# Optimization experiments

Hardware: AMD Instinct MI355X
Metric: run time of the kernel (lower is better)

Reference implementation:

```python
import jax, jax.numpy as jnp
import numpy as np

N, E, D_IN, D_OUT = 50000, 300000, 256, 256
BN_EPS = 1e-5


def ccorr(a, b):
    # circular correlation: irfft(conj(rfft(a)) * rfft(b))
    return jnp.fft.irfft(jnp.conj(jnp.fft.rfft(a, axis=-1)) * jnp.fft.rfft(b, axis=-1), n=a.shape[-1], axis=-1)


def setup_inputs() -> dict:
    key = jax.random.key(0)
    ks = jax.random.split(key, 8)
    return {
        "node_ft": jax.random.normal(ks[0], (N, D_IN), dtype=jnp.float32),
        "edge_ft": jax.random.normal(ks[1], (E, D_IN), dtype=jnp.float32),
        "norm": jax.random.uniform(ks[2], (N, 1), dtype=jnp.float32),
        "w_loop": jax.random.normal(ks[3], (D_IN, D_OUT), dtype=jnp.float32) * (1.414 / np.sqrt(D_IN)),
        "w_in": jax.random.normal(ks[4], (D_IN, D_OUT), dtype=jnp.float32) * (1.414 / np.sqrt(D_IN)),
        "loop_rel": jax.random.normal(ks[5], (1, D_IN), dtype=jnp.float32),
        "w_bias": jnp.zeros((D_OUT,), dtype=jnp.float32),
        "bn_gamma": jnp.ones((D_OUT,), dtype=jnp.float32),
        "bn_beta": jnp.zeros((D_OUT,), dtype=jnp.float32),
        "src": jax.random.randint(ks[6], (E,), 0, N, dtype=jnp.int32),
        "dst": jax.random.randint(ks[7], (E,), 0, N, dtype=jnp.int32),
    }


def reference(node_ft, edge_ft, norm, w_loop, w_in, loop_rel, w_bias, bn_gamma, bn_beta, src, dst):
    n_nodes = node_ft.shape[0]
    # self-loop message: ccorr(ft, loop_rel) @ w_loop  [N, d_out]
    loop_msg = ccorr(node_ft, loop_rel) @ w_loop
    # per-edge message: ccorr(src_ft, edge_ft) @ w_in  [E, d_out]
    msg = ccorr(node_ft[src], edge_ft) @ w_in
    # scatter-sum aggregation then norm multiply (apply_func)
    agg = jax.ops.segment_sum(msg, dst, num_segments=n_nodes) * norm
    h = agg + w_bias + loop_msg
    # BatchNorm1d (training mode: batch stats, biased variance)
    mean = jnp.mean(h, axis=0)
    var = jnp.var(h, axis=0)
    h = (h - mean) * jax.lax.rsqrt(var + BN_EPS) * bn_gamma + bn_beta
    return jnp.tanh(h)
```

## Files before the change

kernel.cpp:

```cpp
#include <hip/hip_runtime.h>
#include <hip/hip_bf16.h>

#define NN 50000
#define EE 300000
#define BN_EPS 1e-5f
#define NFW 288
#define TWOPI_256 0.024543692606170259f

typedef __attribute__((ext_vector_type(8))) _Float16 half8;
typedef __attribute__((ext_vector_type(2))) _Float16 half2v;
typedef __attribute__((ext_vector_type(4))) float f32x4;
#define MFMA16F __builtin_amdgcn_mfma_f32_16x16x32_f16

__device__ __align__(16) _Float16 g_NF[(size_t)NN * NFW];
__device__ float g_Wle[256 * 256];
__device__ __align__(16) unsigned short g_FB[8 * 20 * 64 * 8];
__device__ __align__(16) unsigned short g_CB[9 * 16 * 64 * 8];
__device__ __align__(16) unsigned short g_WLEB[8 * 16 * 64 * 8];
__device__ int g_hist[NN];
__device__ int g_off[NN];
__device__ int g_cursor[NN];
__device__ int g_perm[EE];
__device__ int g_bsum[128];
__device__ int g_bbase[128];

__device__ __forceinline__ void atomAddF(float* p, float v) { unsafeAtomicAdd(p, v); }

__device__ __forceinline__ unsigned short f2hu(float x) {
    union { _Float16 f; unsigned short u; } c;
    c.f = (_Float16)x;
    return c.u;
}

__device__ __forceinline__ void stage_write(char* A, const float4* stg, int t) {
#pragma unroll
    for (int q = 0; q < 8; ++q) {
        int idx = q * 512 + t;
        int row = idx >> 6, c4 = idx & 63;
        union { _Float16 f[4]; ushort4 u; } r;
        r.f[0] = (_Float16)stg[q].x; r.f[1] = (_Float16)stg[q].y;
        r.f[2] = (_Float16)stg[q].z; r.f[3] = (_Float16)stg[q].w;
        int ks = c4 >> 3;
        int off = ((row >> 4) * 8 + ks) * 1024 +
                  ((((((c4 >> 1) & 3) << 4) | (row & 15)) * 16) ^ (ks << 4)) +
                  (c4 & 1) * 8;
        *(ushort4*)(A + off) = r.u;
    }
}

__global__ __launch_bounds__(512) void hist_kernel(const int* __restrict__ dst, int E) {
    int e = blockIdx.x * 512 + threadIdx.x;
    if (e < E) atomicAdd(&g_hist[dst[e]], 1);
}

__global__ __launch_bounds__(512) void scanA_kernel(int N) {
    __shared__ int arr[512];
    int t = threadIdx.x, b = blockIdx.x * 512 + t;
    int cnt = (b < N) ? g_hist[b] : 0;
    arr[t] = cnt;
    __syncthreads();
#pragma unroll
    for (int off = 1; off < 512; off <<= 1) {
        int v = (t >= off) ? arr[t - off] : 0;
        __syncthreads();
        arr[t] += v;
        __syncthreads();
    }
    if (b < N) g_off[b] = arr[t] - cnt;
    if (t == 511) g_bsum[blockIdx.x] = arr[511];
}

__global__ __launch_bounds__(128) void scanB_kernel(int nblk) {
    __shared__ int arr[128];
    int t = threadIdx.x;
    int v0 = (t < nblk) ? g_bsum[t] : 0;
    arr[t] = v0;
    __syncthreads();
#pragma unroll
    for (int off = 1; off < 128; off <<= 1) {
        int v = (t >= off) ? arr[t - off] : 0;
        __syncthreads();
        arr[t] += v;
        __syncthreads();
    }
    if (t < nblk) g_bbase[t] = arr[t] - v0;
}

__global__ __launch_bounds__(512) void scanC_kernel(int N) {
    int b = blockIdx.x * 512 + threadIdx.x;
    if (b < N) {
        int v = g_off[b] + g_bbase[blockIdx.x];
        g_off[b] = v;
        g_cursor[b] = v;
    }
}

__global__ __launch_bounds__(512) void perm_kernel(const int* __restrict__ dst, int E) {
    int e = blockIdx.x * 512 + threadIdx.x;
    if (e < E) {
        int pos = atomicAdd(&g_cursor[dst[e]], 1);
        g_perm[pos] = e;
    }
}

__global__ __launch_bounds__(256) void wle_kernel(
    const float* __restrict__ loop_rel, const float* __restrict__ w_loop,
    float* __restrict__ W_le) {
    __shared__ float lr[256];
    const int d = threadIdx.x, j = blockIdx.x;
    lr[d] = loop_rel[d];
    __syncthreads();
    float acc = 0.f;
#pragma unroll 4
    for (int k = 0; k < 256; ++k)
        acc = fmaf(lr[(j + k) & 255], w_loop[k * 256 + d], acc);
    W_le[j * 256 + d] = acc;
}

__global__ __launch_bounds__(512) void fb_pack() {
    int b = blockIdx.x, ks = b / 20, nt = b % 20;
    int t = threadIdx.x, lane = t >> 3, e = t & 7;
    int k = 32 * ks + 8 * (lane >> 4) + e;
    int r2 = nt * 16 + (lane & 15);
    float val = 0.f;
    if (r2 < 258) {
        int f = r2 >> 1;
        int m = (f * k) & 255;
        float s, c;
        sincosf((float)m * TWOPI_256, &s, &c);
        val = (r2 & 1) ? -s : c;
    }
    g_FB[((ks * 20 + nt) * 64 + lane) * 8 + e] = f2hu(val);
}

__global__ __launch_bounds__(512) void cb_pack(const float* __restrict__ w_in) {
    __shared__ float ct[256], st[256];
    int t = threadIdx.x;
    if (t < 256) {
        float s, c;
        sincosf((float)t * TWOPI_256, &s, &c);
        ct[t] = c; st[t] = s;
    }
    __syncthreads();
    int b = blockIdx.x, ks = b / 16, nt = b % 16;
    int lane = t >> 3, e = t & 7;
    int kk = 32 * ks + 8 * (lane >> 4) + e;
    int d = nt * 16 + (lane & 15);
    float val = 0.f;
    if (kk < 258) {
        int f = kk >> 1;
        float cf = (f == 0 || f == 128) ? (1.f / 256.f) : (2.f / 256.f);
        const float* tab = (kk & 1) ? st : ct;
        float sgn = (kk & 1) ? -1.f : 1.f;
        float acc = 0.f;
        for (int k = 0; k < 256; ++k)
            acc = fmaf(tab[(f * k) & 255], w_in[k * 256 + d], acc);
        val = cf * sgn * acc;
    }
    g_CB[((ks * 16 + nt) * 64 + lane) * 8 + e] = f2hu(val);
}

__global__ __launch_bounds__(512) void wleb_pack() {
    int b = blockIdx.x, ks = b / 16, nt = b % 16;
    int t = threadIdx.x, lane = t >> 3, e = t & 7;
    int k = 32 * ks + 8 * (lane >> 4) + e;
    int d = nt * 16 + (lane & 15);
    g_WLEB[((ks * 16 + nt) * 64 + lane) * 8 + e] = f2hu(g_Wle[k * 256 + d]);
}

__global__ __launch_bounds__(512, 4) void nfloop_kernel(
    const float* __restrict__ node_ft, const float* __restrict__ w_bias,
    float* __restrict__ out, int N) {
    __shared__ char smem[32768];
    unsigned short* A = (unsigned short*)smem;
    const int t = threadIdx.x;
    const long long r0 = (long long)blockIdx.x * 64;
    {
        float4 stg[8];
#pragma unroll
        for (int q = 0; q < 8; ++q) {
            int idx = q * 512 + t;
            long long gr = r0 + (idx >> 6);
            if (gr >= N) gr = N - 1;
            stg[q] = ((const float4*)node_ft)[gr * 64 + (idx & 63)];
        }
        stage_write(smem, stg, t);
    }
    __syncthreads();

    const int lane = t & 63, w = t >> 6;
    const int mw = w >> 2, nw = w & 3;
    const int l15 = lane & 15, lg = lane >> 4;

    {
        f32x4 acc[2][5] = {};
#pragma unroll
        for (int ks = 0; ks < 8; ++ks) {
            half8 a0 = *(const half8*)((char*)A + ((2 * mw + 0) * 8 + ks) * 1024 + ((lane * 16) ^ (ks << 4)));
            half8 a1 = *(const half8*)((char*)A + ((2 * mw + 1) * 8 + ks) * 1024 + ((lane * 16) ^ (ks << 4)));
#pragma unroll
            for (int j = 0; j < 4; ++j) {
                int tn = nw + 4 * j;
                half8 bf = *(const half8*)(g_FB + ((size_t)(ks * 20 + tn) * 64 + lane) * 8);
                acc[0][j] = MFMA16F(a0, bf, acc[0][j], 0, 0, 0);
                acc[1][j] = MFMA16F(a1, bf, acc[1][j], 0, 0, 0);
            }
            if (nw == 0) {
                half8 bf = *(const half8*)(g_FB + ((size_t)(ks * 20 + 16) * 64 + lane) * 8);
                acc[0][4] = MFMA16F(a0, bf, acc[0][4], 0, 0, 0);
                acc[1][4] = MFMA16F(a1, bf, acc[1][4], 0, 0, 0);
            }
        }
#pragma unroll
        for (int mt = 0; mt < 2; ++mt)
#pragma unroll
            for (int j = 0; j < 5; ++j) {
                int tn = nw + 4 * j;
                if (tn > 16 || (j == 4 && nw != 0)) continue;
                int r2 = tn * 16 + l15;
#pragma unroll
                for (int r = 0; r < 4; ++r) {
                    long long gr = r0 + (2 * mw + mt) * 16 + lg * 4 + r;
                    if (gr < N && r2 < 258)
                        g_NF[gr * NFW + r2] = (_Float16)acc[mt][j][r];
                }
            }
    }
    {
        f32x4 acc[2][4] = {};
#pragma unroll
        for (int ks = 0; ks < 8; ++ks) {
            half8 a0 = *(const half8*)((char*)A + ((2 * mw + 0) * 8 + ks) * 1024 + ((lane * 16) ^ (ks << 4)));
            half8 a1 = *(const half8*)((char*)A + ((2 * mw + 1) * 8 + ks) * 1024 + ((lane * 16) ^ (ks << 4)));
#pragma unroll
            for (int j = 0; j < 4; ++j) {
                half8 bf = *(const half8*)(g_WLEB + ((size_t)(ks * 16 + 4 * nw + j) * 64 + lane) * 8);
                acc[0][j] = MFMA16F(a0, bf, acc[0][j], 0, 0, 0);
                acc[1][j] = MFMA16F(a1, bf, acc[1][j], 0, 0, 0);
            }
        }
#pragma unroll
        for (int j = 0; j < 4; ++j) {
            const int col = (4 * nw + j) * 16 + l15;
            const float bj = w_bias[col];
#pragma unroll
            for (int mt = 0; mt < 2; ++mt)
#pragma unroll
                for (int r = 0; r < 4; ++r) {
                    long long gr = r0 + (2 * mw + mt) * 16 + lg * 4 + r;
                    if (gr < N)
                        out[gr * 256 + col] = acc[mt][j][r] + bj;
                }
        }
    }
}

__global__ __launch_bounds__(512, 4) void edge_kernel(
    const float* __restrict__ edge_ft, const float* __restrict__ norm,
    const int* __restrict__ src, const int* __restrict__ dst,
    float* __restrict__ agg, int E) {
    __shared__ char smem[36864 + 512];
    unsigned short* A = (unsigned short*)smem;
    unsigned short* Z = (unsigned short*)smem;
    int* sdd = (int*)(smem + 36864);
    float* snrm = (float*)(smem + 36864 + 256);

    const int t = threadIdx.x;
    const long long ebase = (long long)blockIdx.x * 64;
    const int lane = t & 63, w = t >> 6;
    const int mw = w >> 2, nw = w & 3;
    const int l15 = lane & 15, lg = lane >> 4;
    const bool odd = (l15 & 1);

    int srcv[2][4];
#pragma unroll
    for (int mt = 0; mt < 2; ++mt)
#pragma unroll
        for (int r = 0; r < 4; ++r) {
            long long ge = ebase + (2 * mw + mt) * 16 + lg * 4 + r;
            if (ge >= E) ge = E - 1;
            srcv[mt][r] = src[g_perm[ge]];
        }

    if (t < 64) {
        long long ge = ebase + t;
        if (ge >= E) ge = E - 1;
        int d = dst[g_perm[ge]];
        sdd[t] = d;
        snrm[t] = norm[d];
    }

    float4 stg[8];
#pragma unroll
    for (int q = 0; q < 8; ++q) {
        long long ge = ebase + q * 8 + (t >> 6);
        if (ge >= E) ge = E - 1;
        stg[q] = ((const float4*)edge_ft)[(long long)g_perm[ge] * 64 + (t & 63)];
    }

    unsigned int pf[2][5][4];
#pragma unroll
    for (int mt = 0; mt < 2; ++mt)
#pragma unroll
        for (int j = 0; j < 5; ++j) {
            int tn = nw + 4 * j;
            if (tn >= 17) continue;
            int r2 = tn * 16 + l15;
            if (r2 < 258) {
#pragma unroll
                for (int r = 0; r < 4; ++r)
                    pf[mt][j][r] = *(const unsigned int*)(g_NF +
                        (long long)srcv[mt][r] * NFW + (r2 & ~1));
            }
        }
    stage_write(smem, stg, t);
    __syncthreads();

    f32x4 acc1[2][5] = {};
#pragma unroll
    for (int ks = 0; ks < 8; ++ks) {
        half8 a0 = *(const half8*)((char*)A + ((2 * mw + 0) * 8 + ks) * 1024 + ((lane * 16) ^ (ks << 4)));
        half8 a1 = *(const half8*)((char*)A + ((2 * mw + 1) * 8 + ks) * 1024 + ((lane * 16) ^ (ks << 4)));
#pragma unroll
        for (int j = 0; j < 4; ++j) {
            int tn = nw + 4 * j;
            half8 bf = *(const half8*)(g_FB + ((size_t)(ks * 20 + tn) * 64 + lane) * 8);
            acc1[0][j] = MFMA16F(a0, bf, acc1[0][j], 0, 0, 0);
            acc1[1][j] = MFMA16F(a1, bf, acc1[1][j], 0, 0, 0);
        }
        if (nw == 0) {
            half8 bf = *(const half8*)(g_FB + ((size_t)(ks * 20 + 16) * 64 + lane) * 8);
            acc1[0][4] = MFMA16F(a0, bf, acc1[0][4], 0, 0, 0);
            acc1[1][4] = MFMA16F(a1, bf, acc1[1][4], 0, 0, 0);
        }
    }
    __syncthreads();

#pragma unroll
    for (int mt = 0; mt < 2; ++mt) {
        int tm = 2 * mw + mt;
#pragma unroll
        for (int j = 0; j < 5; ++j) {
            int tn = nw + 4 * j;
            if (tn >= 18) continue;
            int r2 = tn * 16 + l15;
#pragma unroll
            for (int r = 0; r < 4; ++r) {
                int e = tm * 16 + lg * 4 + r;
                float z = 0.f;
                if (r2 < 258) {
                    float own = acc1[mt][j][r];
                    float oth = __shfl_xor(own, 1);
                    union { unsigned int u; half2v h; } cv;
                    cv.u = pf[mt][j][r];
                    float br = (float)cv.h[0], bi = (float)cv.h[1];
                    z = odd ? (br * own - bi * oth) : (br * own + bi * oth);
                }
                int ksz = r2 >> 5;
                int off = ((e >> 4) * 9 + ksz) * 1024 +
                          ((((((r2 >> 3) & 3) << 4) | (e & 15)) * 16) ^ (ksz << 4)) +
                          (r2 & 7) * 2;
                *(unsigned short*)((char*)Z + off) = f2hu(z);
            }
        }
    }
    __syncthreads();

    f32x4 acc2[2][4] = {};
#pragma unroll
    for (int ks = 0; ks < 9; ++ks) {
        half8 a0 = *(const half8*)((char*)Z + ((2 * mw + 0) * 9 + ks) * 1024 + ((lane * 16) ^ (ks << 4)));
        half8 a1 = *(const half8*)((char*)Z + ((2 * mw + 1) * 9 + ks) * 1024 + ((lane * 16) ^ (ks << 4)));
#pragma unroll
        for (int j = 0; j < 4; ++j) {
            half8 bf = *(const half8*)(g_CB + ((size_t)(ks * 16 + 4 * nw + j) * 64 + lane) * 8);
            acc2[0][j] = MFMA16F(a0, bf, acc2[0][j], 0, 0, 0);
            acc2[1][j] = MFMA16F(a1, bf, acc2[1][j], 0, 0, 0);
        }
    }

#pragma unroll
    for (int mt = 0; mt < 2; ++mt) {
        const int e0 = (2 * mw + mt) * 16 + lg * 4;
        const bool v0 = ebase + e0 < E, v1 = ebase + e0 + 1 < E;
        const bool v2 = ebase + e0 + 2 < E, v3 = ebase + e0 + 3 < E;
        const int d0 = sdd[e0], d1 = sdd[e0 + 1], d2 = sdd[e0 + 2], d3 = sdd[e0 + 3];
        const float n0 = snrm[e0], n1 = snrm[e0 + 1], n2 = snrm[e0 + 2], n3 = snrm[e0 + 3];
        const bool uni = v3 && (d0 == d1) && (d1 == d2) && (d2 == d3);
        const bool p01 = v1 && (d0 == d1);
        const bool p23 = v3 && (d2 == d3);
#pragma unroll
        for (int j = 0; j < 4; ++j) {
            const int col = (4 * nw + j) * 16 + l15;
            float x0 = acc2[mt][j][0] * n0, x1 = acc2[mt][j][1] * n1;
            float x2 = acc2[mt][j][2] * n2, x3 = acc2[mt][j][3] * n3;
            if (uni) {
                atomAddF(agg + (long long)d0 * 256 + col, (x0 + x1) + (x2 + x3));
            } else {
                if (p01) atomAddF(agg + (long long)d0 * 256 + col, x0 + x1);
                else {
                    if (v0) atomAddF(agg + (long long)d0 * 256 + col, x0);
                    if (v1) atomAddF(agg + (long long)d1 * 256 + col, x1);
                }
                if (p23) atomAddF(agg + (long long)d2 * 256 + col, x2 + x3);
                else {
                    if (v2) atomAddF(agg + (long long)d2 * 256 + col, x2);
                    if (v3) atomAddF(agg + (long long)d3 * 256 + col, x3);
                }
            }
        }
    }
}

__global__ __launch_bounds__(256) void stats_kernel(
    const float* __restrict__ h, float* __restrict__ s1g,
    float* __restrict__ s2g, long long tot4) {
    __shared__ float s1l[256], s2l[256];
    const int t = threadIdx.x;
    s1l[t] = 0.f;
    s2l[t] = 0.f;
    __syncthreads();
    const int dg = t & 63;
    float a1[4] = {0.f, 0.f, 0.f, 0.f}, a2[4] = {0.f, 0.f, 0.f, 0.f};
    const long long stride = (long long)gridDim.x * 256;
    for (long long i4 = (long long)blockIdx.x * 256 + t; i4 < tot4; i4 += stride) {
        float4 v = ((const float4*)h)[i4];
        a1[0] += v.x; a2[0] += v.x * v.x;
        a1[1] += v.y; a2[1] += v.y * v.y;
        a1[2] += v.z; a2[2] += v.z * v.z;
        a1[3] += v.w; a2[3] += v.w * v.w;
    }
#pragma unroll
    for (int c = 0; c < 4; ++c) {
        atomicAdd(&s1l[dg * 4 + c], a1[c]);
        atomicAdd(&s2l[dg * 4 + c], a2[c]);
    }
    __syncthreads();
    atomAddF(&s1g[t], s1l[t]);
    atomAddF(&s2g[t], s2l[t]);
}

__global__ __launch_bounds__(256) void finalize_kernel(
    float* __restrict__ out, const float* __restrict__ s1g,
    const float* __restrict__ s2g, const float* __restrict__ gamma,
    const float* __restrict__ beta, int N) {
    long long i4 = (long long)blockIdx.x * blockDim.x + threadIdx.x;
    long long tot = (long long)N * 64;
    if (i4 >= tot) return;
    const int dg = (int)(i4 & 63);
    float4 h = ((float4*)out)[i4];
    const float4 s1 = ((const float4*)s1g)[dg];
    const float4 s2 = ((const float4*)s2g)[dg];
    const float4 g = ((const float4*)gamma)[dg];
    const float4 b = ((const float4*)beta)[dg];
    const float invN = 1.f / (float)N;
    float4 o;
    { float m = s1.x * invN; float v = s2.x * invN - m * m;
      o.x = tanhf(fmaf(h.x - m, rsqrtf(v + BN_EPS) * g.x, b.x)); }
    { float m = s1.y * invN; float v = s2.y * invN - m * m;
      o.y = tanhf(fmaf(h.y - m, rsqrtf(v + BN_EPS) * g.y, b.y)); }
    { float m = s1.z * invN; float v = s2.z * invN - m * m;
      o.z = tanhf(fmaf(h.z - m, rsqrtf(v + BN_EPS) * g.z, b.z)); }
    { float m = s1.w * invN; float v = s2.w * invN - m * m;
      o.w = tanhf(fmaf(h.w - m, rsqrtf(v + BN_EPS) * g.w, b.w)); }
    ((float4*)out)[i4] = o;
}

extern "C" void kernel_launch(void* const* d_in, const int* in_sizes, int n_in,
                              void* d_out, int out_size, void* d_ws, size_t ws_size,
                              hipStream_t stream) {
    const float* node_ft  = (const float*)d_in[0];
    const float* edge_ft  = (const float*)d_in[1];
    const float* norm     = (const float*)d_in[2];
    const float* w_loop   = (const float*)d_in[3];
    const float* w_in     = (const float*)d_in[4];
    const float* loop_rel = (const float*)d_in[5];
    const float* w_bias   = (const float*)d_in[6];
    const float* bn_gamma = (const float*)d_in[7];
    const float* bn_beta  = (const float*)d_in[8];
    const int*   src      = (const int*)d_in[9];
    const int*   dst      = (const int*)d_in[10];

    const int N = in_sizes[2];
    const int E = in_sizes[9];
    float* out = (float*)d_out;

    float* s1g = (float*)d_ws;
    float* s2g = s1g + 256;

    hipMemsetAsync(d_ws, 0, 512 * sizeof(float), stream);

    float* Wle_ptr = nullptr;
    hipGetSymbolAddress((void**)&Wle_ptr, HIP_SYMBOL(g_Wle));
    void* hist_ptr = nullptr;
    hipGetSymbolAddress(&hist_ptr, HIP_SYMBOL(g_hist));
    hipMemsetAsync(hist_ptr, 0, (size_t)N * sizeof(int), stream);

    const int sblk = (N + 511) / 512;
    const int eblk = (E + 511) / 512;

    hist_kernel<<<eblk, 512, 0, stream>>>(dst, E);
    scanA_kernel<<<sblk, 512, 0, stream>>>(N);
    scanB_kernel<<<1, 128, 0, stream>>>(sblk);
    scanC_kernel<<<sblk, 512, 0, stream>>>(N);
    perm_kernel<<<eblk, 512, 0, stream>>>(dst, E);

    wle_kernel<<<256, 256, 0, stream>>>(loop_rel, w_loop, Wle_ptr);
    fb_pack<<<8 * 20, 512, 0, stream>>>();
    cb_pack<<<9 * 16, 512, 0, stream>>>(w_in);
    wleb_pack<<<8 * 16, 512, 0, stream>>>();

    nfloop_kernel<<<(N + 63) / 64, 512, 0, stream>>>(node_ft, w_bias, out, N);
    edge_kernel<<<(E + 63) / 64, 512, 0, stream>>>(edge_ft, norm, src, dst, out, E);
    stats_kernel<<<256, 256, 0, stream>>>(out, s1g, s2g, (long long)N * 64);
    finalize_kernel<<<(int)(((long long)N * 64 + 255) / 256), 256, 0, stream>>>(
        out, s1g, s2g, bn_gamma, bn_beta, N);
}
```

Measured before the change: 451.1 us.

## Replace atomic scatter with fp16 message buffer and CSR segmented reduction

The edge kernel now reads edge features and src in their natural order, so loads are coalesced. It writes each fp16 message row to a dst-sorted slot found by a position kernel. A new reduction kernel sums each node's messages in CSR order, applies norm, adds the result to the self-loop output and accumulates the BatchNorm statistics in the same pass, which removes the float atomics and the separate stats pass. In exchange it writes and reads a 150 MB fp16 intermediate, loses precision from rounding messages to fp16, and makes the scattered row writes uncoalesced.

```diff
diff --git a/kernel.cpp b/kernel.cpp
--- a/kernel.cpp
+++ b/kernel.cpp
@@ -13,14 +13,15 @@
 #define MFMA16F __builtin_amdgcn_mfma_f32_16x16x32_f16
 
 __device__ __align__(16) _Float16 g_NF[(size_t)NN * NFW];
+__device__ __align__(16) _Float16 g_MSG[(size_t)EE * 256];
 __device__ float g_Wle[256 * 256];
 __device__ __align__(16) unsigned short g_FB[8 * 20 * 64 * 8];
 __device__ __align__(16) unsigned short g_CB[9 * 16 * 64 * 8];
 __device__ __align__(16) unsigned short g_WLEB[8 * 16 * 64 * 8];
 __device__ int g_hist[NN];
-__device__ int g_off[NN];
+__device__ int g_off[NN + 1];
 __device__ int g_cursor[NN];
-__device__ int g_perm[EE];
+__device__ int g_pos[EE];
 __device__ int g_bsum[128];
 __device__ int g_bbase[128];
 
@@ -92,14 +93,15 @@
         int v = g_off[b] + g_bbase[blockIdx.x];
         g_off[b] = v;
         g_cursor[b] = v;
-    }
-}
-
-__global__ __launch_bounds__(512) void perm_kernel(const int* __restrict__ dst, int E) {
+        if (b == N - 1) g_off[N] = v + g_hist[b];
+    }
+}
+
+__global__ __launch_bounds__(512) void pos_kernel(const int* __restrict__ dst, int E) {
     int e = blockIdx.x * 512 + threadIdx.x;
     if (e < E) {
         int pos = atomicAdd(&g_cursor[dst[e]], 1);
-        g_perm[pos] = e;
+        g_pos[e] = pos;
     }
 }
 
@@ -255,15 +257,11 @@
     }
 }
 
-__global__ __launch_bounds__(512, 4) void edge_kernel(
-    const float* __restrict__ edge_ft, const float* __restrict__ norm,
-    const int* __restrict__ src, const int* __restrict__ dst,
-    float* __restrict__ agg, int E) {
-    __shared__ char smem[36864 + 512];
+__global__ __launch_bounds__(512, 4) void edgeA_kernel(
+    const float* __restrict__ edge_ft, const int* __restrict__ src, int E) {
+    __shared__ char smem[36864];
     unsigned short* A = (unsigned short*)smem;
     unsigned short* Z = (unsigned short*)smem;
-    int* sdd = (int*)(smem + 36864);
-    float* snrm = (float*)(smem + 36864 + 256);
 
     const int t = threadIdx.x;
     const long long ebase = (long long)blockIdx.x * 64;
@@ -272,48 +270,27 @@
     const int l15 = lane & 15, lg = lane >> 4;
     const bool odd = (l15 & 1);
 
-    int srcv[2][4];
+    int srcv[2][4], posv[2][4];
 #pragma unroll
     for (int mt = 0; mt < 2; ++mt)
 #pragma unroll
         for (int r = 0; r < 4; ++r) {
             long long ge = ebase + (2 * mw + mt) * 16 + lg * 4 + r;
             if (ge >= E) ge = E - 1;
-            srcv[mt][r] = src[g_perm[ge]];
-        }
-
-    if (t < 64) {
-        long long ge = ebase + t;
-        if (ge >= E) ge = E - 1;
-        int d = dst[g_perm[ge]];
-        sdd[t] = d;
-        snrm[t] = norm[d];
-    }
-
-    float4 stg[8];
-#pragma unroll
-    for (int q = 0; q < 8; ++q) {
-        long long ge = ebase + q * 8 + (t >> 6);
-        if (ge >= E) ge = E - 1;
-        stg[q] = ((const float4*)edge_ft)[(long long)g_perm[ge] * 64 + (t & 63)];
-    }
-
-    unsigned int pf[2][5][4];
-#pragma unroll
-    for (int mt = 0; mt < 2; ++mt)
-#pragma unroll
-        for (int j = 0; j < 5; ++j) {
-            int tn = nw + 4 * j;
-            if (tn >= 17) continue;
-            int r2 = tn * 16 + l15;
-            if (r2 < 258) {
-#pragma unroll
-                for (int r = 0; r < 4; ++r)
-                    pf[mt][j][r] = *(const unsigned int*)(g_NF +
-                        (long long)srcv[mt][r] * NFW + (r2 & ~1));
-            }
-        }
-    stage_write(smem, stg, t);
+            srcv[mt][r] = src[ge];
+            posv[mt][r] = g_pos[ge];
+        }
+
+    {
+        float4 stg[8];
+#pragma unroll
+        for (int q = 0; q < 8; ++q) {
+            long long ge = ebase + q * 8 + (t >> 6);
+            if (ge >= E) ge = E - 1;
+            stg[q] = ((const float4*)edge_ft)[ge * 64 + (t & 63)];
+        }
+        stage_write(smem, stg, t);
+    }
     __syncthreads();
 
     f32x4 acc1[2][5] = {};
@@ -352,7 +329,8 @@
                     float own = acc1[mt][j][r];
                     float oth = __shfl_xor(own, 1);
                     union { unsigned int u; half2v h; } cv;
-                    cv.u = pf[mt][j][r];
+                    cv.u = *(const unsigned int*)(g_NF +
+                        (long long)srcv[mt][r] * NFW + (r2 & ~1));
                     float br = (float)cv.h[0], bi = (float)cv.h[1];
                     z = odd ? (br * own - bi * oth) : (br * own + bi * oth);
                 }
@@ -380,64 +358,74 @@
     }
 
 #pragma unroll
-    for (int mt = 0; mt < 2; ++mt) {
-        const int e0 = (2 * mw + mt) * 16 + lg * 4;
-        const bool v0 = ebase + e0 < E, v1 = ebase + e0 + 1 < E;
-        const bool v2 = ebase + e0 + 2 < E, v3 = ebase + e0 + 3 < E;
-        const int d0 = sdd[e0], d1 = sdd[e0 + 1], d2 = sdd[e0 + 2], d3 = sdd[e0 + 3];
-        const float n0 = snrm[e0], n1 = snrm[e0 + 1], n2 = snrm[e0 + 2], n3 = snrm[e0 + 3];
-        const bool uni = v3 && (d0 == d1) && (d1 == d2) && (d2 == d3);
-        const bool p01 = v1 && (d0 == d1);
-        const bool p23 = v3 && (d2 == d3);
-#pragma unroll
-        for (int j = 0; j < 4; ++j) {
-            const int col = (4 * nw + j) * 16 + l15;
-            float x0 = acc2[mt][j][0] * n0, x1 = acc2[mt][j][1] * n1;
-            float x2 = acc2[mt][j][2] * n2, x3 = acc2[mt][j][3] * n3;
-            if (uni) {
-                atomAddF(agg + (long long)d0 * 256 + col, (x0 + x1) + (x2 + x3));
-            } else {
-                if (p01) atomAddF(agg + (long long)d0 * 256 + col, x0 + x1);
-                else {
-                    if (v0) atomAddF(agg + (long long)d0 * 256 + col, x0);
-                    if (v1) atomAddF(agg + (long long)d1 * 256 + col, x1);
-                }
-                if (p23) atomAddF(agg + (long long)d2 * 256 + col, x2 + x3);
-                else {
-                    if (v2) atomAddF(agg + (long long)d2 * 256 + col, x2);
-                    if (v3) atomAddF(agg + (long long)d3 * 256 + col, x3);
-                }
+    for (int mt = 0; mt < 2; ++mt)
+#pragma unroll
+        for (int r = 0; r < 4; ++r) {
+            long long ge = ebase + (2 * mw + mt) * 16 + lg * 4 + r;
+            if (ge < E) {
+                _Float16* mrow = g_MSG + (size_t)posv[mt][r] * 256;
+#pragma unroll
+                for (int j = 0; j < 4; ++j)
+                    mrow[(4 * nw + j) * 16 + l15] = (_Float16)acc2[mt][j][r];
             }
         }
-    }
-}
-
-__global__ __launch_bounds__(256) void stats_kernel(
-    const float* __restrict__ h, float* __restrict__ s1g,
-    float* __restrict__ s2g, long long tot4) {
+}
+
+__global__ __launch_bounds__(512) void reduceB_kernel(
+    const float* __restrict__ norm, float* __restrict__ out,
+    float* __restrict__ s1g, float* __restrict__ s2g, int N) {
     __shared__ float s1l[256], s2l[256];
     const int t = threadIdx.x;
-    s1l[t] = 0.f;
-    s2l[t] = 0.f;
-    __syncthreads();
-    const int dg = t & 63;
+    if (t < 256) { s1l[t] = 0.f; s2l[t] = 0.f; }
+    __syncthreads();
+    const int w = t >> 6, lane = t & 63;
     float a1[4] = {0.f, 0.f, 0.f, 0.f}, a2[4] = {0.f, 0.f, 0.f, 0.f};
-    const long long stride = (long long)gridDim.x * 256;
-    for (long long i4 = (long long)blockIdx.x * 256 + t; i4 < tot4; i4 += stride) {
-        float4 v = ((const float4*)h)[i4];
-        a1[0] += v.x; a2[0] += v.x * v.x;
-        a1[1] += v.y; a2[1] += v.y * v.y;
-        a1[2] += v.z; a2[2] += v.z * v.z;
-        a1[3] += v.w; a2[3] += v.w * v.w;
+
+#pragma unroll 1
+    for (int i = 0; i < 8; ++i) {
+        int n = blockIdx.x * 64 + w * 8 + i;
+        if (n >= N) break;
+        const int s = g_off[n], e2 = g_off[n + 1];
+        const float nrm = norm[n];
+        float4 ms = make_float4(0.f, 0.f, 0.f, 0.f);
+        int i2 = s;
+        for (; i2 + 1 < e2; i2 += 2) {
+            half2v p0 = *(const half2v*)(g_MSG + (size_t)i2 * 256 + lane * 4);
+            half2v p1 = *(const half2v*)(g_MSG + (size_t)i2 * 256 + lane * 4 + 2);
+            half2v q0 = *(const half2v*)(g_MSG + (size_t)(i2 + 1) * 256 + lane * 4);
+            half2v q1 = *(const half2v*)(g_MSG + (size_t)(i2 + 1) * 256 + lane * 4 + 2);
+            ms.x += (float)p0[0] + (float)q0[0];
+            ms.y += (float)p0[1] + (float)q0[1];
+            ms.z += (float)p1[0] + (float)q1[0];
+            ms.w += (float)p1[1] + (float)q1[1];
+        }
+        if (i2 < e2) {
+            half2v p0 = *(const half2v*)(g_MSG + (size_t)i2 * 256 + lane * 4);
+            half2v p1 = *(const half2v*)(g_MSG + (size_t)i2 * 256 + lane * 4 + 2);
+            ms.x += (float)p0[0]; ms.y += (float)p0[1];
+            ms.z += (float)p1[0]; ms.w += (float)p1[1];
+        }
+        float4 hv = ((const float4*)out)[(size_t)n * 64 + lane];
+        hv.x = fmaf(ms.x, nrm, hv.x);
+        hv.y = fmaf(ms.y, nrm, hv.y);
+        hv.z = fmaf(ms.z, nrm, hv.z);
+        hv.w = fmaf(ms.w, nrm, hv.w);
+        ((float4*)out)[(size_t)n * 64 + lane] = hv;
+        a1[0] += hv.x; a2[0] += hv.x * hv.x;
+        a1[1] += hv.y; a2[1] += hv.y * hv.y;
+        a1[2] += hv.z; a2[2] += hv.z * hv.z;
+        a1[3] += hv.w; a2[3] += hv.w * hv.w;
     }
 #pragma unroll
     for (int c = 0; c < 4; ++c) {
-        atomicAdd(&s1l[dg * 4 + c], a1[c]);
-        atomicAdd(&s2l[dg * 4 + c], a2[c]);
-    }
-    __syncthreads();
-    atomAddF(&s1g[t], s1l[t]);
-    atomAddF(&s2g[t], s2l[t]);
+        atomicAdd(&s1l[lane * 4 + c], a1[c]);
+        atomicAdd(&s2l[lane * 4 + c], a2[c]);
+    }
+    __syncthreads();
+    if (t < 256) {
+        atomAddF(&s1g[t], s1l[t]);
+        atomAddF(&s2g[t], s2l[t]);
+    }
 }
 
 __global__ __launch_bounds__(256) void finalize_kernel(
@@ -503,7 +491,7 @@
     scanA_kernel<<<sblk, 512, 0, stream>>>(N);
     scanB_kernel<<<1, 128, 0, stream>>>(sblk);
     scanC_kernel<<<sblk, 512, 0, stream>>>(N);
-    perm_kernel<<<eblk, 512, 0, stream>>>(dst, E);
+    pos_kernel<<<eblk, 512, 0, stream>>>(dst, E);
 
     wle_kernel<<<256, 256, 0, stream>>>(loop_rel, w_loop, Wle_ptr);
     fb_pack<<<8 * 20, 512, 0, stream>>>();
@@ -511,8 +499,8 @@
     wleb_pack<<<8 * 16, 512, 0, stream>>>();
 
     nfloop_kernel<<<(N + 63) / 64, 512, 0, stream>>>(node_ft, w_bias, out, N);
-    edge_kernel<<<(E + 63) / 64, 512, 0, stream>>>(edge_ft, norm, src, dst, out, E);
-    stats_kernel<<<256, 256, 0, stream>>>(out, s1g, s2g, (long long)N * 64);
+    edgeA_kernel<<<(E + 63) / 64, 512, 0, stream>>>(edge_ft, src, E);
+    reduceB_kernel<<<(N + 63) / 64, 512, 0, stream>>>(norm, out, s1g, s2g, N);
     finalize_kernel<<<(int)(((long long)N * 64 + 255) / 256), 256, 0, stream>>>(
         out, s1g, s2g, bn_gamma, bn_beta, N);
 }
```

After: 475.1 us. 1.05x slower.

## Handle Nyquist frequency bin separately with scalar sums instead of extra MFMA tiles

Applied to the files above, without the earlier changes.

The real-FFT Nyquist bin is now computed directly as an alternating-sign wave reduction in fp32, and it is applied as a rank-1 FMA correction with a saved fp32 row of the combined weight. This removes the fifth MFMA column tile in the forward DFT and shrinks the second GEMM's K from 9 to 8 slices. As a result the Z buffer in shared memory gets smaller and the occupancy hint rises from 4 to 6. The source-feature gathers are no longer prefetched into registers before the MFMA and are now loaded at use time, which lowers register pressure but may expose gather latency.

```diff
diff --git a/kernel.cpp b/kernel.cpp
--- a/kernel.cpp
+++ b/kernel.cpp
@@ -14,11 +14,12 @@
 
 __device__ __align__(16) _Float16 g_NF[(size_t)NN * NFW];
 __device__ float g_Wle[256 * 256];
+__device__ float g_C256[256];
 __device__ __align__(16) unsigned short g_FB[8 * 20 * 64 * 8];
 __device__ __align__(16) unsigned short g_CB[9 * 16 * 64 * 8];
 __device__ __align__(16) unsigned short g_WLEB[8 * 16 * 64 * 8];
 __device__ int g_hist[NN];
-__device__ int g_off[NN];
+__device__ int g_off[NN + 1];
 __device__ int g_cursor[NN];
 __device__ int g_perm[EE];
 __device__ int g_bsum[128];
@@ -48,6 +49,12 @@
     }
 }
 
+__device__ __forceinline__ float waveSum(float v) {
+#pragma unroll
+    for (int d = 1; d < 64; d <<= 1) v += __shfl_xor(v, d);
+    return v;
+}
+
 __global__ __launch_bounds__(512) void hist_kernel(const int* __restrict__ dst, int E) {
     int e = blockIdx.x * 512 + threadIdx.x;
     if (e < E) atomicAdd(&g_hist[dst[e]], 1);
@@ -92,6 +99,7 @@
         int v = g_off[b] + g_bbase[blockIdx.x];
         g_off[b] = v;
         g_cursor[b] = v;
+        if (b == N - 1) g_off[N] = v + g_hist[b];
     }
 }
 
@@ -157,6 +165,7 @@
             acc = fmaf(tab[(f * k) & 255], w_in[k * 256 + d], acc);
         val = cf * sgn * acc;
     }
+    if (kk == 256) g_C256[d] = val;
     g_CB[((ks * 16 + nt) * 64 + lane) * 8 + e] = f2hu(val);
 }
 
@@ -174,6 +183,7 @@
     __shared__ char smem[32768];
     unsigned short* A = (unsigned short*)smem;
     const int t = threadIdx.x;
+    const int wv = t >> 6;
     const long long r0 = (long long)blockIdx.x * 64;
     {
         float4 stg[8];
@@ -184,16 +194,24 @@
             if (gr >= N) gr = N - 1;
             stg[q] = ((const float4*)node_ft)[gr * 64 + (idx & 63)];
         }
+#pragma unroll
+        for (int q = 0; q < 8; ++q) {
+            float c = stg[q].x - stg[q].y + stg[q].z - stg[q].w;
+            c = waveSum(c);
+            int row = q * 8 + wv;
+            if ((t & 63) == 0 && r0 + row < N)
+                g_NF[(r0 + row) * NFW + 256] = (_Float16)c;
+        }
         stage_write(smem, stg, t);
     }
     __syncthreads();
 
-    const int lane = t & 63, w = t >> 6;
-    const int mw = w >> 2, nw = w & 3;
+    const int lane = t & 63;
+    const int mw = wv >> 2, nw = wv & 3;
     const int l15 = lane & 15, lg = lane >> 4;
 
     {
-        f32x4 acc[2][5] = {};
+        f32x4 acc[2][4] = {};
 #pragma unroll
         for (int ks = 0; ks < 8; ++ks) {
             half8 a0 = *(const half8*)((char*)A + ((2 * mw + 0) * 8 + ks) * 1024 + ((lane * 16) ^ (ks << 4)));
@@ -205,24 +223,16 @@
                 acc[0][j] = MFMA16F(a0, bf, acc[0][j], 0, 0, 0);
                 acc[1][j] = MFMA16F(a1, bf, acc[1][j], 0, 0, 0);
             }
-            if (nw == 0) {
-                half8 bf = *(const half8*)(g_FB + ((size_t)(ks * 20 + 16) * 64 + lane) * 8);
-                acc[0][4] = MFMA16F(a0, bf, acc[0][4], 0, 0, 0);
-                acc[1][4] = MFMA16F(a1, bf, acc[1][4], 0, 0, 0);
-            }
         }
 #pragma unroll
         for (int mt = 0; mt < 2; ++mt)
 #pragma unroll
-            for (int j = 0; j < 5; ++j) {
-                int tn = nw + 4 * j;
-                if (tn > 16 || (j == 4 && nw != 0)) continue;
-                int r2 = tn * 16 + l15;
+            for (int j = 0; j < 4; ++j) {
+                int r2 = (nw + 4 * j) * 16 + l15;
 #pragma unroll
                 for (int r = 0; r < 4; ++r) {
                     long long gr = r0 + (2 * mw + mt) * 16 + lg * 4 + r;
-                    if (gr < N && r2 < 258)
-                        g_NF[gr * NFW + r2] = (_Float16)acc[mt][j][r];
+                    if (gr < N) g_NF[gr * NFW + r2] = (_Float16)acc[mt][j][r];
                 }
             }
     }
@@ -255,68 +265,54 @@
     }
 }
 
-__global__ __launch_bounds__(512, 4) void edge_kernel(
+__global__ __launch_bounds__(512, 6) void edge_kernel(
     const float* __restrict__ edge_ft, const float* __restrict__ norm,
     const int* __restrict__ src, const int* __restrict__ dst,
     float* __restrict__ agg, int E) {
-    __shared__ char smem[36864 + 512];
+    __shared__ char smem[32768 + 1024];
     unsigned short* A = (unsigned short*)smem;
     unsigned short* Z = (unsigned short*)smem;
-    int* sdd = (int*)(smem + 36864);
-    float* snrm = (float*)(smem + 36864 + 256);
+    int*   sdd  = (int*)(smem + 32768);
+    float* snrm = (float*)(smem + 32768 + 256);
+    int*   ssrc = (int*)(smem + 32768 + 512);
+    float* nyq  = (float*)(smem + 32768 + 768);
 
     const int t = threadIdx.x;
     const long long ebase = (long long)blockIdx.x * 64;
-    const int lane = t & 63, w = t >> 6;
-    const int mw = w >> 2, nw = w & 3;
+    const int lane = t & 63, wv = t >> 6;
+    const int mw = wv >> 2, nw = wv & 3;
     const int l15 = lane & 15, lg = lane >> 4;
     const bool odd = (l15 & 1);
-
-    int srcv[2][4];
-#pragma unroll
-    for (int mt = 0; mt < 2; ++mt)
-#pragma unroll
-        for (int r = 0; r < 4; ++r) {
-            long long ge = ebase + (2 * mw + mt) * 16 + lg * 4 + r;
-            if (ge >= E) ge = E - 1;
-            srcv[mt][r] = src[g_perm[ge]];
-        }
 
     if (t < 64) {
         long long ge = ebase + t;
         if (ge >= E) ge = E - 1;
-        int d = dst[g_perm[ge]];
+        int p = g_perm[ge];
+        int d = dst[p];
         sdd[t] = d;
         snrm[t] = norm[d];
-    }
-
-    float4 stg[8];
-#pragma unroll
-    for (int q = 0; q < 8; ++q) {
-        long long ge = ebase + q * 8 + (t >> 6);
-        if (ge >= E) ge = E - 1;
-        stg[q] = ((const float4*)edge_ft)[(long long)g_perm[ge] * 64 + (t & 63)];
-    }
-
-    unsigned int pf[2][5][4];
-#pragma unroll
-    for (int mt = 0; mt < 2; ++mt)
-#pragma unroll
-        for (int j = 0; j < 5; ++j) {
-            int tn = nw + 4 * j;
-            if (tn >= 17) continue;
-            int r2 = tn * 16 + l15;
-            if (r2 < 258) {
-#pragma unroll
-                for (int r = 0; r < 4; ++r)
-                    pf[mt][j][r] = *(const unsigned int*)(g_NF +
-                        (long long)srcv[mt][r] * NFW + (r2 & ~1));
-            }
-        }
-    stage_write(smem, stg, t);
-    __syncthreads();
-
-    f32x4 acc1[2][5] = {};
+        ssrc[t] = src[p];
+    }
+
+    {
+        float4 stg[8];
+#pragma unroll
+        for (int q = 0; q < 8; ++q) {
+            long long ge = ebase + q * 8 + wv;
+            if (ge >= E) ge = E - 1;
+            stg[q] = ((const float4*)edge_ft)[(long long)g_perm[ge] * 64 + lane];
+        }
+#pragma unroll
+        for (int q = 0; q < 8; ++q) {
+            float c = stg[q].x - stg[q].y + stg[q].z - stg[q].w;
+            c = waveSum(c);
+            if (lane == 0) nyq[q * 8 + wv] = c;
+        }
+        stage_write(smem, stg, t);
+    }
+    __syncthreads();
+
+    f32x4 acc1[2][4] = {};
 #pragma unroll
     for (int ks = 0; ks < 8; ++ks) {
         half8 a0 = *(const half8*)((char*)A + ((2 * mw + 0) * 8 + ks) * 1024 + ((lane * 16) ^ (ks << 4)));
@@ -328,36 +324,30 @@
             acc1[0][j] = MFMA16F(a0, bf, acc1[0][j], 0, 0, 0);
             acc1[1][j] = MFMA16F(a1, bf, acc1[1][j], 0, 0, 0);
         }
-        if (nw == 0) {
-            half8 bf = *(const half8*)(g_FB + ((size_t)(ks * 20 + 16) * 64 + lane) * 8);
-            acc1[0][4] = MFMA16F(a0, bf, acc1[0][4], 0, 0, 0);
-            acc1[1][4] = MFMA16F(a1, bf, acc1[1][4], 0, 0, 0);
-        }
-    }
-    __syncthreads();
+    }
+    __syncthreads();
+
+    if (t < 64)
+        nyq[t] = nyq[t] * (float)g_NF[(size_t)ssrc[t] * NFW + 256];
 
 #pragma unroll
     for (int mt = 0; mt < 2; ++mt) {
         int tm = 2 * mw + mt;
 #pragma unroll
-        for (int j = 0; j < 5; ++j) {
-            int tn = nw + 4 * j;
-            if (tn >= 18) continue;
-            int r2 = tn * 16 + l15;
-#pragma unroll
-            for (int r = 0; r < 4; ++r) {
-                int e = tm * 16 + lg * 4 + r;
-                float z = 0.f;
-                if (r2 < 258) {
-                    float own = acc1[mt][j][r];
-                    float oth = __shfl_xor(own, 1);
-                    union { unsigned int u; half2v h; } cv;
-                    cv.u = pf[mt][j][r];
-                    float br = (float)cv.h[0], bi = (float)cv.h[1];
-                    z = odd ? (br * own - bi * oth) : (br * own + bi * oth);
-                }
+        for (int r = 0; r < 4; ++r) {
+            int e = tm * 16 + lg * 4 + r;
+            const char* nfrow = (const char*)(g_NF + (size_t)ssrc[e] * NFW);
+#pragma unroll
+            for (int j = 0; j < 4; ++j) {
+                int r2 = (nw + 4 * j) * 16 + l15;
+                float own = acc1[mt][j][r];
+                float oth = __shfl_xor(own, 1);
+                union { unsigned int u; half2v h; } cv;
+                cv.u = *(const unsigned int*)(nfrow + (r2 & ~1) * 2);
+                float br = (float)cv.h[0], bi = (float)cv.h[1];
+                float z = odd ? (br * own - bi * oth) : (br * own + bi * oth);
                 int ksz = r2 >> 5;
-                int off = ((e >> 4) * 9 + ksz) * 1024 +
+                int off = (tm * 8 + ksz) * 1024 +
                           ((((((r2 >> 3) & 3) << 4) | (e & 15)) * 16) ^ (ksz << 4)) +
                           (r2 & 7) * 2;
                 *(unsigned short*)((char*)Z + off) = f2hu(z);
@@ -368,15 +358,29 @@
 
     f32x4 acc2[2][4] = {};
 #pragma unroll
-    for (int ks = 0; ks < 9; ++ks) {
-        half8 a0 = *(const half8*)((char*)Z + ((2 * mw + 0) * 9 + ks) * 1024 + ((lane * 16) ^ (ks << 4)));
-        half8 a1 = *(const half8*)((char*)Z + ((2 * mw + 1) * 9 + ks) * 1024 + ((lane * 16) ^ (ks << 4)));
+    for (int ks = 0; ks < 8; ++ks) {
+        half8 a0 = *(const half8*)((char*)Z + ((2 * mw + 0) * 8 + ks) * 1024 + ((lane * 16) ^ (ks << 4)));
+        half8 a1 = *(const half8*)((char*)Z + ((2 * mw + 1) * 8 + ks) * 1024 + ((lane * 16) ^ (ks << 4)));
 #pragma unroll
         for (int j = 0; j < 4; ++j) {
             half8 bf = *(const half8*)(g_CB + ((size_t)(ks * 16 + 4 * nw + j) * 64 + lane) * 8);
             acc2[0][j] = MFMA16F(a0, bf, acc2[0][j], 0, 0, 0);
             acc2[1][j] = MFMA16F(a1, bf, acc2[1][j], 0, 0, 0);
         }
+    }
+    {
+        float c256[4];
+#pragma unroll
+        for (int j = 0; j < 4; ++j) c256[j] = g_C256[(4 * nw + j) * 16 + l15];
+#pragma unroll
+        for (int mt = 0; mt < 2; ++mt)
+#pragma unroll
+            for (int r = 0; r < 4; ++r) {
+                float zn = nyq[(2 * mw + mt) * 16 + lg * 4 + r];
+#pragma unroll
+                for (int j = 0; j < 4; ++j)
+                    acc2[mt][j][r] = fmaf(zn, c256[j], acc2[mt][j][r]);
+            }
     }
 
 #pragma unroll
```

Result: no change. 455.7 us (+1.0%).
